# Optimization experiments

Hardware: AMD Instinct MI355X
Metric: run time of the kernel (lower is better)

The kernel has to match this reference:

```python
import jax, jax.numpy as jnp
import numpy as np
import math

MAX_P = 150
D_MODEL = 128
N_HEADS = 4
D_HEAD = D_MODEL // N_HEADS
D_MLP = 512
D_MEM = 64
VOCAB = MAX_P + 2  # 152
EQ_TOKEN = MAX_P + 1  # 151
B = 65536


def setup_inputs() -> dict:
    key = jax.random.key(0)
    ks = jax.random.split(key, 20)
    s = 1.0 / math.sqrt(D_MODEL)
    inp = {
        "p_val": jax.random.randint(ks[0], (B,), 0, MAX_P),
        "a": jax.random.randint(ks[1], (B,), 0, MAX_P),
        "b": jax.random.randint(ks[2], (B,), 0, MAX_P),
        # embeddings
        "token_embed": jax.random.normal(ks[3], (VOCAB, D_MODEL), jnp.float32),
        "pos_embed": jax.random.normal(ks[4], (5, D_MODEL), jnp.float32),
        # TitansMemory
        "W_mem": jax.random.normal(ks[5], (D_MODEL, D_MEM), jnp.float32) * s,
        "b_mem": jnp.zeros((D_MEM,), jnp.float32),
        "W_sur": jax.random.normal(ks[6], (D_MEM, D_MODEL), jnp.float32) * (1.0 / math.sqrt(D_MEM)),
        "b_sur": jnp.zeros((D_MODEL,), jnp.float32),
        "W_m2r": jax.random.normal(ks[7], (D_MEM, D_MODEL), jnp.float32) * (1.0 / math.sqrt(D_MEM)),
        "b_m2r": jnp.zeros((D_MODEL,), jnp.float32),
        # attention
        "W_Q": jax.random.normal(ks[8], (N_HEADS, D_MODEL, D_HEAD), jnp.float32) * s,
        "W_K": jax.random.normal(ks[9], (N_HEADS, D_MODEL, D_HEAD), jnp.float32) * s,
        "W_V": jax.random.normal(ks[10], (N_HEADS, D_MODEL, D_HEAD), jnp.float32) * s,
        "W_O": jax.random.normal(ks[11], (N_HEADS, D_HEAD, D_MODEL), jnp.float32) * s,
        # MLP
        "W_mlp1": jax.random.normal(ks[12], (D_MODEL, D_MLP), jnp.float32) * s,
        "b_mlp1": jnp.zeros((D_MLP,), jnp.float32),
        "W_mlp2": jax.random.normal(ks[13], (D_MLP, D_MODEL), jnp.float32) * (1.0 / math.sqrt(D_MLP)),
        "b_mlp2": jnp.zeros((D_MODEL,), jnp.float32),
        # unembed
        "W_un": jax.random.normal(ks[14], (D_MODEL, MAX_P), jnp.float32) * s,
        "b_un": jnp.zeros((MAX_P,), jnp.float32),
    }
    return inp


def reference(p_val, a, b, token_embed, pos_embed, W_mem, b_mem, W_sur, b_sur,
              W_m2r, b_m2r, W_Q, W_K, W_V, W_O, W_mlp1, b_mlp1, W_mlp2, b_mlp2,
              W_un, b_un):
    eq = jnp.full_like(a, EQ_TOKEN)
    tokens = jnp.stack([p_val, a, b, eq], axis=1)            # [B, 4]
    x = token_embed[tokens] + pos_embed[:4][None, :, :]       # [B, 4, D]

    # Titans memory (test-time update) on the modulus token embedding
    x0 = x[:, 0, :]                                           # [B, D]
    z = jax.nn.silu(x0 @ W_mem + b_mem)                       # [B, d_mem]
    pred_x = z @ W_sur + b_sur                                # [B, D]
    update = jax.nn.silu((x0 - pred_x) @ W_mem)               # [B, d_mem]
    mem = (z + update) @ W_m2r + b_m2r                        # [B, D]
    x = x + mem[:, None, :]

    # attention
    q = jnp.einsum('bsd,hdk->bhsk', x, W_Q)
    k = jnp.einsum('bsd,hdk->bhsk', x, W_K)
    v = jnp.einsum('bsd,hdk->bhsk', x, W_V)
    scores = jnp.einsum('bhsk,bhtk->bhst', q, k) / math.sqrt(D_HEAD)
    pattern = jax.nn.softmax(scores, axis=-1)                 # [B, H, 4, 4]
    attn = jnp.einsum('bhst,bhtk->bhsk', pattern, v)
    attn = jnp.einsum('bhsk,hkm->bsm', attn, W_O)             # [B, 4, D]
    x = x + attn

    # MLP
    x = x + jax.nn.relu(x @ W_mlp1 + b_mlp1) @ W_mlp2 + b_mlp2

    # unembed the '=' position
    logits = x[:, 3, :] @ W_un + b_un                         # [B, max_p]
    return logits
```

## Files before the change

### kernel.cpp

```cpp
#include <hip/hip_runtime.h>

#define D      128
#define DM     64
#define DMLP   512
#define PMAX   150
#define VOC    152
#define EQT    151
#define NBATCH 65536

typedef __attribute__((ext_vector_type(8))) __bf16 bf16x8;
typedef __attribute__((ext_vector_type(4))) float  f32x4;

__device__ __forceinline__ float silu_f(float x){ return x / (1.0f + expf(-x)); }

__device__ __forceinline__ void gl_lds16(const void* g, void* l) {
    __builtin_amdgcn_global_load_lds(
        (const __attribute__((address_space(1))) void*)g,
        (__attribute__((address_space(3))) void*)l, 16, 0, 0);
}

#define OFF_MEMVEC 0
#define OFF_X3BASE 19200
#define OFF_KE     19328
#define OFF_KP     38784
#define OFF_SC     39296
#define OFF_O0     132896
#define OFF_O1     171296
#define OFF_O2     209696
#define OFF_O3     248096
#define OFF_M3B    248352
#define OFF_W1F    257952
#define OFF_W2F    290720
#define OFF_WUF    323488

__global__ void k_P1a(const float* __restrict__ tok, const float* __restrict__ pos,
                      const float* __restrict__ W_mem, const float* __restrict__ b_mem,
                      const float* __restrict__ W_sur, const float* __restrict__ b_sur,
                      const float* __restrict__ W_m2r, const float* __restrict__ b_m2r,
                      const float* __restrict__ W_K,
                      float* __restrict__ memvec, float* __restrict__ x3base,
                      float* __restrict__ KE, float* __restrict__ KP)
{
    int r = blockIdx.x, t = threadIdx.x;
    if (r < 150) {
        int p = r;
        __shared__ float sx0[D], sz[DM], sdiff[D], szu[DM], red4[4][DM], red2[2][D];
        if (t < D) sx0[t] = tok[p*D + t] + pos[t];
        __syncthreads();
        {
            int out = t & 63, seg = t >> 6, k0 = seg*32;
            float acc = 0.f;
            for (int k = 0; k < 32; k++) acc += sx0[k0+k] * W_mem[(k0+k)*DM + out];
            red4[seg][out] = acc;
        }
        __syncthreads();
        if (t < DM) sz[t] = silu_f(b_mem[t] + red4[0][t] + red4[1][t] + red4[2][t] + red4[3][t]);
        __syncthreads();
        {
            int out = t & 127, seg = t >> 7, j0 = seg*32;
            float acc = 0.f;
            for (int j = 0; j < 32; j++) acc += sz[j0+j] * W_sur[(j0+j)*D + out];
            red2[seg][out] = acc;
        }
        __syncthreads();
        if (t < D) sdiff[t] = sx0[t] - (b_sur[t] + red2[0][t] + red2[1][t]);
        __syncthreads();
        {
            int out = t & 63, seg = t >> 6, k0 = seg*32;
            float acc = 0.f;
            for (int k = 0; k < 32; k++) acc += sdiff[k0+k] * W_mem[(k0+k)*DM + out];
            red4[seg][out] = acc;
        }
        __syncthreads();
        if (t < DM) szu[t] = sz[t] + silu_f(red4[0][t] + red4[1][t] + red4[2][t] + red4[3][t]);
        __syncthreads();
        {
            int out = t & 127, seg = t >> 7, j0 = seg*32;
            float acc = 0.f;
            for (int j = 0; j < 32; j++) acc += szu[j0+j] * W_m2r[(j0+j)*D + out];
            red2[seg][out] = acc;
        }
        __syncthreads();
        if (t < D) memvec[p*D + t] = b_m2r[t] + red2[0][t] + red2[1][t];
    } else if (r == 150) {
        if (t < D) x3base[t] = tok[EQT*D + t] + pos[3*D + t];
    } else {
        int idx = r - 151;
        const float* src = (idx < 152) ? (tok + idx*D) : (pos + (idx-152)*D);
        float*       dst = (idx < 152) ? (KE + idx*D)  : (KP + (idx-152)*D);
        __shared__ float s[D], red2[2][D];
        if (t < D) s[t] = src[t];
        __syncthreads();
        {
            int out = t & 127, seg = t >> 7, h = out >> 5, kk = out & 31, d0 = seg*64;
            float acc = 0.f;
            for (int d = 0; d < 64; d++) acc += s[d0+d] * W_K[h*4096 + (d0+d)*32 + kk];
            red2[seg][out] = acc;
        }
        __syncthreads();
        if (t < D) dst[t] = red2[0][t] + red2[1][t];
    }
}

__global__ void k_P2x(const float* __restrict__ memvec, const float* __restrict__ x3base,
                      const float* __restrict__ W_Q, const float* __restrict__ W_V,
                      const float* __restrict__ W_O,
                      const float* __restrict__ KE, const float* __restrict__ KP,
                      const float* __restrict__ tok, const float* __restrict__ pos,
                      const float* __restrict__ W1, const float* __restrict__ W2,
                      const float* __restrict__ WU,
                      float* __restrict__ SC, __bf16* __restrict__ M3B,
                      __bf16* __restrict__ O0, __bf16* __restrict__ O1,
                      __bf16* __restrict__ O2, __bf16* __restrict__ O3,
                      __bf16* __restrict__ W1f, __bf16* __restrict__ W2f, __bf16* __restrict__ WUf)
{
    int r = blockIdx.x, t = threadIdx.x;
    if (r < 300) {
        int p = r >> 1, half = r & 1;
        __shared__ float sMem[D], sIn[D], sQ3[D], sMV[D], redM[2][D];
        if (t < D) { float m = memvec[p*D + t]; sMem[t] = m; sIn[t] = m + x3base[t]; }
        __syncthreads();
        if (t < D) {
            int h = t >> 5, k = t & 31;
            float acc = 0.f;
            for (int d = 0; d < D; d++) acc += sIn[d] * W_Q[h*4096 + d*32 + k];
            sQ3[t] = acc;
        } else {
            int c = t - D; int h = c >> 5, k = c & 31;
            float acc = 0.f;
            for (int d = 0; d < D; d++) acc += sMem[d] * W_V[h*4096 + d*32 + k];
            sMV[c] = acc;
        }
        __syncthreads();
        const float scale = 0.17677669529663687f;
        for (int ii = t; ii < 312; ii += 256) {
            int i = half*312 + ii;
            int v = i >> 2, h = i & 3;
            const float4* qh = (const float4*)(sQ3 + h*32);
            float4 s4 = {0.f, 0.f, 0.f, 0.f};
            if (v < 152) {
                const float4* ke = (const float4*)(KE + v*D + h*32);
                #pragma unroll
                for (int k = 0; k < 8; k++) {
                    float4 q = qh[k], e = ke[k];
                    s4.x += q.x*e.x; s4.y += q.y*e.y; s4.z += q.z*e.z; s4.w += q.w*e.w;
                }
            } else if (v == 152 || v == 153) {
                const float4* ke = (const float4*)(KE + ((v==152)? p : EQT)*D + h*32);
                const float4* kp = (const float4*)(KP + ((v==152)? 0 : 3)*D + h*32);
                #pragma unroll
                for (int k = 0; k < 8; k++) {
                    float4 q = qh[k], e = ke[k], pp = kp[k];
                    s4.x += q.x*(e.x+pp.x); s4.y += q.y*(e.y+pp.y);
                    s4.z += q.z*(e.z+pp.z); s4.w += q.w*(e.w+pp.w);
                }
            } else {
                const float4* kp = (const float4*)(KP + ((v==154)?1:2)*D + h*32);
                #pragma unroll
                for (int k = 0; k < 8; k++) {
                    float4 q = qh[k], pp = kp[k];
                    s4.x += q.x*pp.x; s4.y += q.y*pp.y; s4.z += q.z*pp.z; s4.w += q.w*pp.w;
                }
            }
            SC[p*624 + i] = (s4.x + s4.y + s4.z + s4.w) * scale;
        }
        if (half == 0) {
            {
                int out = t & 127, seg = t >> 7, c0 = seg*64;
                float acc = 0.f;
                for (int c = 0; c < 64; c++) acc += sMV[c0+c] * W_O[(c0+c)*D + out];
                redM[seg][out] = acc;
            }
            __syncthreads();
            if (t < D) M3B[p*D + t] = (__bf16)(sIn[t] + redM[0][t] + redM[1][t]);
        }
        return;
    }
    int rr = r - 300;
    if (rr < 451) {
        int idx = rr;
        int tt, v; __bf16* outp;
        if (idx < 150)      { tt = 0; v = idx;       outp = O0 + v*512; }
        else if (idx < 300) { tt = 1; v = idx - 150; outp = O1 + (idx-150)*512; }
        else if (idx < 450) { tt = 2; v = idx - 300; outp = O2 + (idx-300)*512; }
        else                { tt = 3; v = EQT;       outp = O3; }
        __shared__ float sTP[D], sv[D], red2[2][D];
        if (t < D) sTP[t] = tok[v*D + t] + pos[tt*D + t];
        __syncthreads();
        {
            int out = t & 127, seg = t >> 7, h = out >> 5, kk = out & 31, d0 = seg*64;
            float acc = 0.f;
            for (int d = 0; d < 64; d++) acc += sTP[d0+d] * W_V[h*4096 + (d0+d)*32 + kk];
            red2[seg][out] = acc;
        }
        __syncthreads();
        if (t < D) sv[t] = red2[0][t] + red2[1][t];
        __syncthreads();
        #pragma unroll
        for (int i = 0; i < 2; i++) {
            int c = t + i*256;
            int h = c >> 7, m = c & 127;
            float acc = 0.f;
            for (int k = 0; k < 32; k++) acc += sv[h*32 + k] * W_O[h*4096 + k*128 + m];
            outp[c] = (__bf16)acc;
        }
    } else if (rr < 483) {
        int f = (rr-451)*256 + t;
        int l = f & 63, kb = (f>>6) & 3, nb = f >> 8;
        int k0 = kb*32 + (l>>4)*8, n = nb*16 + (l&15);
        #pragma unroll
        for (int j = 0; j < 8; j++) W1f[f*8 + j] = (__bf16)W1[(k0+j)*DMLP + n];
    } else if (rr < 515) {
        int f = (rr-483)*256 + t;
        int l = f & 63, g = f >> 6;
        int nb = g & 7, kb = g >> 3;
        int k0 = kb*32 + (l>>4)*8, n = nb*16 + (l&15);
        #pragma unroll
        for (int j = 0; j < 8; j++) W2f[f*8 + j] = (__bf16)W2[(k0+j)*D + n];
    } else {
        int f = (rr-515)*256 + t;
        int l = f & 63, kb = (f>>6) & 3, nb = f >> 8;
        int k0 = kb*32 + (l>>4)*8, n = nb*16 + (l&15);
        #pragma unroll
        for (int j = 0; j < 8; j++) WUf[f*8 + j] = (__bf16)((n < 150) ? WU[(k0+j)*150 + n] : 0.f);
    }
}

__global__ __launch_bounds__(256, 4) void k_fused(
    const int* __restrict__ p_val, const int* __restrict__ a_tok, const int* __restrict__ b_tok,
    const float* __restrict__ SC, const __bf16* __restrict__ O0, const __bf16* __restrict__ O1,
    const __bf16* __restrict__ O2, const __bf16* __restrict__ O3g, const __bf16* __restrict__ M3B,
    const __bf16* __restrict__ W1f, const __bf16* __restrict__ W2f, const __bf16* __restrict__ WUf,
    const float* __restrict__ b1, const float* __restrict__ b2, const float* __restrict__ bun,
    float* __restrict__ out)
{
    __shared__ __align__(16) char smem[39936];
    char* sX3 = smem + 16384;
    float* sB1 = (float*)(smem + 37888);

    int tid = threadIdx.x;
    int wv = tid >> 6, l = tid & 63, lr = l & 15, quad = l >> 4;
    int tbase = blockIdx.x * 64 + wv * 16;

    const char* gW1 = (const char*)W1f;
    const char* gW2 = (const char*)W2f;

    gl_lds16(gW1 + tid*16,       smem + tid*16);
    gl_lds16(gW1 + (tid+256)*16, smem + (tid+256)*16);
    sB1[tid] = b1[tid]; sB1[tid+256] = b1[tid+256];

    {
        int s = tid >> 2, h = tid & 3;
        int gs = blockIdx.x * 64 + s;
        int p = p_val[gs], ta = a_tok[gs], tb = b_tok[gs];

        float wloc[4];
        {
            const float* SCp = SC + p*624;
            float sc0 = SCp[608 + h];
            float sc3 = SCp[612 + h];
            float sc1 = SCp[ta*4 + h] + SCp[616 + h];
            float sc2 = SCp[tb*4 + h] + SCp[620 + h];
            float mx = fmaxf(fmaxf(sc0, sc1), fmaxf(sc2, sc3));
            float e0 = expf(sc0-mx), e1 = expf(sc1-mx), e2 = expf(sc2-mx), e3 = expf(sc3-mx);
            float inv = 1.f / (e0 + e1 + e2 + e3);
            wloc[0] = e0*inv; wloc[1] = e1*inv; wloc[2] = e2*inv; wloc[3] = e3*inv;
        }
        float w[16];
        #pragma unroll
        for (int j = 0; j < 4; j++) w[h*4 + j] = wloc[j];
        #pragma unroll
        for (int m = 1; m < 4; m++) {
            int oh = h ^ m;
            #pragma unroll
            for (int j = 0; j < 4; j++) w[oh*4 + j] = __shfl_xor(wloc[j], m);
        }

        const bf16x8* m3v = (const bf16x8*)(M3B + p*128);
        const bf16x8* t0  = (const bf16x8*)(O0 + p*512);
        const bf16x8* t1  = (const bf16x8*)(O1 + ta*512);
        const bf16x8* t2  = (const bf16x8*)(O2 + tb*512);
        const bf16x8* t3  = (const bf16x8*)O3g;
        #pragma unroll
        for (int jj = 0; jj < 4; jj++) {
            int c8 = h*4 + jj;
            bf16x8 mv = m3v[c8];
            float v[8];
            #pragma unroll
            for (int e = 0; e < 8; e++) v[e] = (float)mv[e];
            #pragma unroll
            for (int hh = 0; hh < 4; hh++) {
                int o8 = hh*16 + c8;
                bf16x8 e0 = t0[o8], e1 = t1[o8], e2 = t2[o8], e3 = t3[o8];
                float w0 = w[hh*4+0], w1 = w[hh*4+1], w2 = w[hh*4+2], w3 = w[hh*4+3];
                #pragma unroll
                for (int e = 0; e < 8; e++)
                    v[e] += w0*(float)e0[e] + w1*(float)e1[e] + w2*(float)e2[e] + w3*(float)e3[e];
            }
            bf16x8 st;
            #pragma unroll
            for (int e = 0; e < 8; e++) st[e] = (__bf16)v[e];
            *(bf16x8*)(sX3 + s*256 + ((c8*16) ^ ((s&7)<<4))) = st;
        }
    }
    asm volatile("s_waitcnt lgkmcnt(0)" ::: "memory");
    __builtin_amdgcn_sched_barrier(0);

    bf16x8 a[4];
    {
        int arow = wv*16 + lr;
        #pragma unroll
        for (int kb = 0; kb < 4; kb++)
            a[kb] = *(const bf16x8*)(sX3 + arow*256 + ((kb*64 + quad*16) ^ ((lr&7)<<4)));
    }
    __syncthreads();
    gl_lds16(gW2 + tid*16,       smem + 16384 + tid*16);
    gl_lds16(gW2 + (tid+256)*16, smem + 16384 + (tid+256)*16);
    __syncthreads();

    char* sPanH = smem + 32768 + wv*1280;

    f32x4 acc2[8];
    #pragma unroll
    for (int i = 0; i < 8; i++) acc2[i] = (f32x4){0.f, 0.f, 0.f, 0.f};

    for (int cc = 0; cc < 16; cc++) {
        int pb = cc & 1;
        char* w1b = smem + pb*8192;
        char* w2b = smem + 16384 + pb*8192;
        if (cc < 15) {
            const char* g1 = gW1 + (cc+1)*8192;
            const char* g2 = gW2 + (cc+1)*8192;
            char* d1 = smem + (pb^1)*8192;
            char* d2 = smem + 16384 + (pb^1)*8192;
            gl_lds16(g1 + tid*16,       d1 + tid*16);
            gl_lds16(g1 + (tid+256)*16, d1 + (tid+256)*16);
            gl_lds16(g2 + tid*16,       d2 + tid*16);
            gl_lds16(g2 + (tid+256)*16, d2 + (tid+256)*16);
        }
        #pragma unroll
        for (int nbl = 0; nbl < 2; nbl++) {
            float bv = sB1[cc*32 + nbl*16 + lr];
            f32x4 acc = (f32x4){bv, bv, bv, bv};
            #pragma unroll
            for (int kb = 0; kb < 4; kb++) {
                bf16x8 w1 = *(const bf16x8*)(w1b + ((nbl*4 + kb)*64 + l)*16);
                acc = __builtin_amdgcn_mfma_f32_16x16x32_bf16(a[kb], w1, acc, 0, 0, 0);
            }
            #pragma unroll
            for (int r = 0; r < 4; r++)
                *(__bf16*)(sPanH + (((quad*4 + r)*40) + nbl*16 + lr)*2) = (__bf16)fmaxf(acc[r], 0.f);
        }
        asm volatile("s_waitcnt lgkmcnt(0)" ::: "memory");
        __builtin_amdgcn_sched_barrier(0);
        {
            bf16x8 h = *(const bf16x8*)(sPanH + (lr*40 + quad*8)*2);
            #pragma unroll
            for (int nb2 = 0; nb2 < 8; nb2++) {
                bf16x8 w2 = *(const bf16x8*)(w2b + (nb2*64 + l)*16);
                acc2[nb2] = __builtin_amdgcn_mfma_f32_16x16x32_bf16(h, w2, acc2[nb2], 0, 0, 0);
            }
        }
        __syncthreads();
    }

    #pragma unroll
    for (int nb2 = 0; nb2 < 8; nb2++) {
        int kb = nb2 >> 1;
        bf16x8 bi;
        #pragma unroll
        for (int j = 0; j < 8; j++)
            bi[j] = (kb*32 + quad*8 + j == nb2*16 + lr) ? (__bf16)1.0f : (__bf16)0.0f;
        acc2[nb2] = __builtin_amdgcn_mfma_f32_16x16x32_bf16(a[kb], bi, acc2[nb2], 0, 0, 0);
    }

    #pragma unroll
    for (int nb2 = 0; nb2 < 8; nb2++) {
        int n = nb2*16 + lr;
        float bv = b2[n];
        #pragma unroll
        for (int r = 0; r < 4; r++) {
            float v = acc2[nb2][r] + bv;
            int row = wv*16 + quad*4 + r;
            *(__bf16*)(smem + row*256 + ((n*2) ^ ((row&7)<<4))) = (__bf16)v;
        }
    }
    asm volatile("s_waitcnt lgkmcnt(0)" ::: "memory");
    __builtin_amdgcn_sched_barrier(0);
    bf16x8 au[4];
    {
        int arow = wv*16 + lr;
        #pragma unroll
        for (int kb = 0; kb < 4; kb++)
            au[kb] = *(const bf16x8*)(smem + arow*256 + ((kb*64 + quad*16) ^ ((lr&7)<<4)));
    }

    const char* gWU = (const char*)WUf;
    char* sWU = smem + 16384;
    #pragma unroll
    for (int q = 0; q < 3; q++) {
        __syncthreads();
        if (q < 2) {
            const char* g = gWU + q*16384;
            gl_lds16(g + tid*16,       sWU + tid*16);
            gl_lds16(g + (tid+256)*16, sWU + (tid+256)*16);
            gl_lds16(g + (tid+512)*16, sWU + (tid+512)*16);
            gl_lds16(g + (tid+768)*16, sWU + (tid+768)*16);
        } else {
            const char* g = gWU + 32768;
            gl_lds16(g + tid*16,       sWU + tid*16);
            gl_lds16(g + (tid+256)*16, sWU + (tid+256)*16);
        }
        __syncthreads();
        int ntn = (q < 2) ? 4 : 2;
        for (int ntl = 0; ntl < ntn; ntl++) {
            int nt = q*4 + ntl;
            int n = nt*16 + lr;
            float bv = (n < 150) ? bun[n] : 0.f;
            f32x4 acc = (f32x4){bv, bv, bv, bv};
            #pragma unroll
            for (int kb = 0; kb < 4; kb++) {
                bf16x8 wu = *(const bf16x8*)(sWU + ((ntl*4 + kb)*64 + l)*16);
                acc = __builtin_amdgcn_mfma_f32_16x16x32_bf16(au[kb], wu, acc, 0, 0, 0);
            }
            if (n < 150) {
                #pragma unroll
                for (int r = 0; r < 4; r++) {
                    int rowg = tbase + quad*4 + r;
                    out[rowg*150 + n] = acc[r];
                }
            }
        }
    }
}

extern "C" void kernel_launch(void* const* d_in, const int* in_sizes, int n_in,
                              void* d_out, int out_size, void* d_ws, size_t ws_size,
                              hipStream_t stream) {
    const int*   p_val = (const int*)d_in[0];
    const int*   a_tok = (const int*)d_in[1];
    const int*   b_tok = (const int*)d_in[2];
    const float* tok   = (const float*)d_in[3];
    const float* pos   = (const float*)d_in[4];
    const float* W_mem = (const float*)d_in[5];
    const float* b_mem = (const float*)d_in[6];
    const float* W_sur = (const float*)d_in[7];
    const float* b_sur = (const float*)d_in[8];
    const float* W_m2r = (const float*)d_in[9];
    const float* b_m2r = (const float*)d_in[10];
    const float* W_Q   = (const float*)d_in[11];
    const float* W_K   = (const float*)d_in[12];
    const float* W_V   = (const float*)d_in[13];
    const float* W_O   = (const float*)d_in[14];
    const float* W1    = (const float*)d_in[15];
    const float* b1    = (const float*)d_in[16];
    const float* W2    = (const float*)d_in[17];
    const float* b2    = (const float*)d_in[18];
    const float* WU    = (const float*)d_in[19];
    const float* bun   = (const float*)d_in[20];
    float* out = (float*)d_out;

    float* ws = (float*)d_ws;
    float* memvec = ws + OFF_MEMVEC;
    float* x3base = ws + OFF_X3BASE;
    float* KE     = ws + OFF_KE;
    float* KP     = ws + OFF_KP;
    float* SC     = ws + OFF_SC;
    __bf16* O0    = (__bf16*)(ws + OFF_O0);
    __bf16* O1    = (__bf16*)(ws + OFF_O1);
    __bf16* O2    = (__bf16*)(ws + OFF_O2);
    __bf16* O3    = (__bf16*)(ws + OFF_O3);
    __bf16* M3B   = (__bf16*)(ws + OFF_M3B);
    __bf16* W1f   = (__bf16*)(ws + OFF_W1F);
    __bf16* W2f   = (__bf16*)(ws + OFF_W2F);
    __bf16* WUf   = (__bf16*)(ws + OFF_WUF);

    k_P1a<<<307, 256, 0, stream>>>(tok, pos, W_mem, b_mem, W_sur, b_sur, W_m2r, b_m2r,
                                   W_K, memvec, x3base, KE, KP);
    k_P2x<<<825, 256, 0, stream>>>(memvec, x3base, W_Q, W_V, W_O, KE, KP,
                                   tok, pos, W1, W2, WU,
                                   SC, M3B, O0, O1, O2, O3, W1f, W2f, WUf);
    k_fused<<<NBATCH/64, 256, 0, stream>>>(p_val, a_tok, b_tok, SC, O0, O1, O2, O3, M3B,
                                           W1f, W2f, WUf, b1, b2, bun, out);
}
```

Before: 169.4 us.

## Process two row groups per wave to reuse staged weights across 128-row tiles

Each block now handles 128 batch rows instead of 64, and each wave computes two 16-row MFMA groups that share every W1, W2 and W_un fragment read from LDS. This halves the number of blocks and the per-row global-to-LDS weight streaming, and the first W2 and unembed chunks are prefetched earlier. The cost is roughly doubled LDS (about 76 KB) and more accumulator registers, with launch bounds relaxed to 2 blocks per CU, which lowers occupancy.

```diff
diff --git a/kernel.cpp b/kernel.cpp
--- a/kernel.cpp
+++ b/kernel.cpp
@@ -226,7 +226,7 @@
     }
 }
 
-__global__ __launch_bounds__(256, 4) void k_fused(
+__global__ __launch_bounds__(256, 2) void k_fused(
     const int* __restrict__ p_val, const int* __restrict__ a_tok, const int* __restrict__ b_tok,
     const float* __restrict__ SC, const __bf16* __restrict__ O0, const __bf16* __restrict__ O1,
     const __bf16* __restrict__ O2, const __bf16* __restrict__ O3g, const __bf16* __restrict__ M3B,
@@ -234,24 +234,28 @@
     const float* __restrict__ b1, const float* __restrict__ b2, const float* __restrict__ bun,
     float* __restrict__ out)
 {
-    __shared__ __align__(16) char smem[39936];
-    char* sX3 = smem + 16384;
-    float* sB1 = (float*)(smem + 37888);
+    __shared__ __align__(16) char smem[77824];
+    char*  sX3 = smem + 45056;
+    float* sB1 = (float*)(smem + 43008);
 
     int tid = threadIdx.x;
     int wv = tid >> 6, l = tid & 63, lr = l & 15, quad = l >> 4;
-    int tbase = blockIdx.x * 64 + wv * 16;
+    int tbase = blockIdx.x * 128 + wv * 32;
 
     const char* gW1 = (const char*)W1f;
     const char* gW2 = (const char*)W2f;
 
     gl_lds16(gW1 + tid*16,       smem + tid*16);
     gl_lds16(gW1 + (tid+256)*16, smem + (tid+256)*16);
+    gl_lds16(gW2 + tid*16,       smem + 16384 + tid*16);
+    gl_lds16(gW2 + (tid+256)*16, smem + 16384 + (tid+256)*16);
     sB1[tid] = b1[tid]; sB1[tid+256] = b1[tid+256];
 
-    {
-        int s = tid >> 2, h = tid & 3;
-        int gs = blockIdx.x * 64 + s;
+    #pragma unroll
+    for (int ss = 0; ss < 2; ss++) {
+        int sl = l >> 2, h = l & 3;
+        int row = wv*32 + ss*16 + sl;
+        int gs = blockIdx.x * 128 + row;
         int p = p_val[gs], ta = a_tok[gs], tb = b_tok[gs];
 
         float wloc[4];
@@ -300,29 +304,29 @@
             bf16x8 st;
             #pragma unroll
             for (int e = 0; e < 8; e++) st[e] = (__bf16)v[e];
-            *(bf16x8*)(sX3 + s*256 + ((c8*16) ^ ((s&7)<<4))) = st;
+            *(bf16x8*)(sX3 + row*256 + ((c8*16) ^ ((row&7)<<4))) = st;
         }
     }
     asm volatile("s_waitcnt lgkmcnt(0)" ::: "memory");
     __builtin_amdgcn_sched_barrier(0);
 
-    bf16x8 a[4];
-    {
-        int arow = wv*16 + lr;
+    bf16x8 a[2][4];
+    #pragma unroll
+    for (int rg = 0; rg < 2; rg++) {
+        int arow = wv*32 + rg*16 + lr;
         #pragma unroll
         for (int kb = 0; kb < 4; kb++)
-            a[kb] = *(const bf16x8*)(sX3 + arow*256 + ((kb*64 + quad*16) ^ ((lr&7)<<4)));
+            a[rg][kb] = *(const bf16x8*)(sX3 + arow*256 + ((kb*64 + quad*16) ^ ((lr&7)<<4)));
     }
     __syncthreads();
-    gl_lds16(gW2 + tid*16,       smem + 16384 + tid*16);
-    gl_lds16(gW2 + (tid+256)*16, smem + 16384 + (tid+256)*16);
-    __syncthreads();
-
-    char* sPanH = smem + 32768 + wv*1280;
-
-    f32x4 acc2[8];
-    #pragma unroll
-    for (int i = 0; i < 8; i++) acc2[i] = (f32x4){0.f, 0.f, 0.f, 0.f};
+
+    char* sPanH = smem + 32768 + wv*2560;
+
+    f32x4 acc2[2][8];
+    #pragma unroll
+    for (int rg = 0; rg < 2; rg++)
+        #pragma unroll
+        for (int i = 0; i < 8; i++) acc2[rg][i] = (f32x4){0.f, 0.f, 0.f, 0.f};
 
     for (int cc = 0; cc < 16; cc++) {
         int pb = cc & 1;
@@ -341,28 +345,41 @@
         #pragma unroll
         for (int nbl = 0; nbl < 2; nbl++) {
             float bv = sB1[cc*32 + nbl*16 + lr];
-            f32x4 acc = (f32x4){bv, bv, bv, bv};
+            f32x4 accA = (f32x4){bv, bv, bv, bv};
+            f32x4 accB = (f32x4){bv, bv, bv, bv};
             #pragma unroll
             for (int kb = 0; kb < 4; kb++) {
                 bf16x8 w1 = *(const bf16x8*)(w1b + ((nbl*4 + kb)*64 + l)*16);
-                acc = __builtin_amdgcn_mfma_f32_16x16x32_bf16(a[kb], w1, acc, 0, 0, 0);
-            }
-            #pragma unroll
-            for (int r = 0; r < 4; r++)
-                *(__bf16*)(sPanH + (((quad*4 + r)*40) + nbl*16 + lr)*2) = (__bf16)fmaxf(acc[r], 0.f);
+                accA = __builtin_amdgcn_mfma_f32_16x16x32_bf16(a[0][kb], w1, accA, 0, 0, 0);
+                accB = __builtin_amdgcn_mfma_f32_16x16x32_bf16(a[1][kb], w1, accB, 0, 0, 0);
+            }
+            #pragma unroll
+            for (int r = 0; r < 4; r++) {
+                *(__bf16*)(sPanH + (((quad*4 + r)*40)      + nbl*16 + lr)*2) = (__bf16)fmaxf(accA[r], 0.f);
+                *(__bf16*)(sPanH + (((16 + quad*4 + r)*40) + nbl*16 + lr)*2) = (__bf16)fmaxf(accB[r], 0.f);
+            }
         }
         asm volatile("s_waitcnt lgkmcnt(0)" ::: "memory");
         __builtin_amdgcn_sched_barrier(0);
         {
-            bf16x8 h = *(const bf16x8*)(sPanH + (lr*40 + quad*8)*2);
+            bf16x8 h0 = *(const bf16x8*)(sPanH + ((lr)*40      + quad*8)*2);
+            bf16x8 h1 = *(const bf16x8*)(sPanH + ((16 + lr)*40 + quad*8)*2);
             #pragma unroll
             for (int nb2 = 0; nb2 < 8; nb2++) {
                 bf16x8 w2 = *(const bf16x8*)(w2b + (nb2*64 + l)*16);
-                acc2[nb2] = __builtin_amdgcn_mfma_f32_16x16x32_bf16(h, w2, acc2[nb2], 0, 0, 0);
-            }
-        }
-        __syncthreads();
-    }
+                acc2[0][nb2] = __builtin_amdgcn_mfma_f32_16x16x32_bf16(h0, w2, acc2[0][nb2], 0, 0, 0);
+                acc2[1][nb2] = __builtin_amdgcn_mfma_f32_16x16x32_bf16(h1, w2, acc2[1][nb2], 0, 0, 0);
+            }
+        }
+        __syncthreads();
+    }
+
+    const char* gWU = (const char*)WUf;
+    char* sWU = smem;
+    gl_lds16(gWU + tid*16,       sWU + tid*16);
+    gl_lds16(gWU + (tid+256)*16, sWU + (tid+256)*16);
+    gl_lds16(gWU + (tid+512)*16, sWU + (tid+512)*16);
+    gl_lds16(gWU + (tid+768)*16, sWU + (tid+768)*16);
 
     #pragma unroll
     for (int nb2 = 0; nb2 < 8; nb2++) {
@@ -371,7 +388,8 @@
         #pragma unroll
         for (int j = 0; j < 8; j++)
             bi[j] = (kb*32 + quad*8 + j == nb2*16 + lr) ? (__bf16)1.0f : (__bf16)0.0f;
-        acc2[nb2] = __builtin_amdgcn_mfma_f32_16x16x32_bf16(a[kb], bi, acc2[nb2], 0, 0, 0);
+        acc2[0][nb2] = __builtin_amdgcn_mfma_f32_16x16x32_bf16(a[0][kb], bi, acc2[0][nb2], 0, 0, 0);
+        acc2[1][nb2] = __builtin_amdgcn_mfma_f32_16x16x32_bf16(a[1][kb], bi, acc2[1][nb2], 0, 0, 0);
     }
 
     #pragma unroll
@@ -379,34 +397,36 @@
         int n = nb2*16 + lr;
         float bv = b2[n];
         #pragma unroll
-        for (int r = 0; r < 4; r++) {
-            float v = acc2[nb2][r] + bv;
-            int row = wv*16 + quad*4 + r;
-            *(__bf16*)(smem + row*256 + ((n*2) ^ ((row&7)<<4))) = (__bf16)v;
-        }
+        for (int rg = 0; rg < 2; rg++)
+            #pragma unroll
+            for (int r = 0; r < 4; r++) {
+                float v = acc2[rg][nb2][r] + bv;
+                int row = wv*32 + rg*16 + quad*4 + r;
+                *(__bf16*)(sX3 + row*256 + ((n*2) ^ ((row&7)<<4))) = (__bf16)v;
+            }
     }
     asm volatile("s_waitcnt lgkmcnt(0)" ::: "memory");
     __builtin_amdgcn_sched_barrier(0);
-    bf16x8 au[4];
-    {
-        int arow = wv*16 + lr;
+    bf16x8 au[2][4];
+    #pragma unroll
+    for (int rg = 0; rg < 2; rg++) {
+        int arow = wv*32 + rg*16 + lr;
         #pragma unroll
         for (int kb = 0; kb < 4; kb++)
-            au[kb] = *(const bf16x8*)(smem + arow*256 + ((kb*64 + quad*16) ^ ((lr&7)<<4)));
-    }
-
-    const char* gWU = (const char*)WUf;
-    char* sWU = smem + 16384;
+            au[rg][kb] = *(const bf16x8*)(sX3 + arow*256 + ((kb*64 + quad*16) ^ ((lr&7)<<4)));
+    }
+
     #pragma unroll
     for (int q = 0; q < 3; q++) {
-        __syncthreads();
-        if (q < 2) {
-            const char* g = gWU + q*16384;
+        if (q == 1) {
+            __syncthreads();
+            const char* g = gWU + 16384;
             gl_lds16(g + tid*16,       sWU + tid*16);
             gl_lds16(g + (tid+256)*16, sWU + (tid+256)*16);
             gl_lds16(g + (tid+512)*16, sWU + (tid+512)*16);
             gl_lds16(g + (tid+768)*16, sWU + (tid+768)*16);
-        } else {
+        } else if (q == 2) {
+            __syncthreads();
             const char* g = gWU + 32768;
             gl_lds16(g + tid*16,       sWU + tid*16);
             gl_lds16(g + (tid+256)*16, sWU + (tid+256)*16);
@@ -417,17 +437,19 @@
             int nt = q*4 + ntl;
             int n = nt*16 + lr;
             float bv = (n < 150) ? bun[n] : 0.f;
-            f32x4 acc = (f32x4){bv, bv, bv, bv};
+            f32x4 accU0 = (f32x4){bv, bv, bv, bv};
+            f32x4 accU1 = (f32x4){bv, bv, bv, bv};
             #pragma unroll
             for (int kb = 0; kb < 4; kb++) {
                 bf16x8 wu = *(const bf16x8*)(sWU + ((ntl*4 + kb)*64 + l)*16);
-                acc = __builtin_amdgcn_mfma_f32_16x16x32_bf16(au[kb], wu, acc, 0, 0, 0);
+                accU0 = __builtin_amdgcn_mfma_f32_16x16x32_bf16(au[0][kb], wu, accU0, 0, 0, 0);
+                accU1 = __builtin_amdgcn_mfma_f32_16x16x32_bf16(au[1][kb], wu, accU1, 0, 0, 0);
             }
             if (n < 150) {
                 #pragma unroll
                 for (int r = 0; r < 4; r++) {
-                    int rowg = tbase + quad*4 + r;
-                    out[rowg*150 + n] = acc[r];
+                    out[(tbase +      quad*4 + r)*150 + n] = accU0[r];
+                    out[(tbase + 16 + quad*4 + r)*150 + n] = accU1[r];
                 }
             }
         }
@@ -480,6 +502,6 @@
     k_P2x<<<825, 256, 0, stream>>>(memvec, x3base, W_Q, W_V, W_O, KE, KP,
                                    tok, pos, W1, W2, WU,
                                    SC, M3B, O0, O1, O2, O3, W1f, W2f, WUf);
-    k_fused<<<NBATCH/64, 256, 0, stream>>>(p_val, a_tok, b_tok, SC, O0, O1, O2, O3, M3B,
-                                           W1f, W2f, WUf, b1, b2, bun, out);
+    k_fused<<<NBATCH/128, 256, 0, stream>>>(p_val, a_tok, b_tok, SC, O0, O1, O2, O3, M3B,
+                                            W1f, W2f, WUf, b1, b2, bun, out);
 }
```

New measurement: 176.2 us. 1.04x slower.
